# Optimization experiments

Measured on AMD Instinct MI355X. Metric: run time of the kernel, lower is better.

Reference implementation:

```python
import jax, jax.numpy as jnp
import numpy as np

N = 40000      # nodes
E = 640000     # edges (before self-loops)
G = 64         # graphs in batch
H = 4          # heads
C = 64         # channels per head (graph_hidden_channels)
F_IN = 256     # num_node_features
NHID = 1024
NOUT = 768
NEG_SLOPE = 0.2


def setup_inputs() -> dict:
    key = jax.random.key(0)
    ks = jax.random.split(key, 20)
    s = 0.05
    inp = {
        "x": jax.random.normal(ks[0], (N, F_IN), jnp.float32),
        "edge_index": jax.random.randint(ks[1], (2, E), 0, N, dtype=jnp.int64),
        "batch": jnp.sort(jax.random.randint(ks[2], (N,), 0, G, dtype=jnp.int64)),
        # GATConv 1: in F_IN -> H heads x C
        "W1": jax.random.normal(ks[3], (F_IN, H * C), jnp.float32) * s,
        "as1": jax.random.normal(ks[4], (H, C), jnp.float32) * s,
        "ad1": jax.random.normal(ks[5], (H, C), jnp.float32) * s,
        "b1": jnp.zeros((H * C,), jnp.float32),
        # GATConv 2: in H*C -> H x C
        "W2": jax.random.normal(ks[6], (H * C, H * C), jnp.float32) * s,
        "as2": jax.random.normal(ks[7], (H, C), jnp.float32) * s,
        "ad2": jax.random.normal(ks[8], (H, C), jnp.float32) * s,
        "b2": jnp.zeros((H * C,), jnp.float32),
        # GATConv 3
        "W3": jax.random.normal(ks[9], (H * C, H * C), jnp.float32) * s,
        "as3": jax.random.normal(ks[10], (H, C), jnp.float32) * s,
        "ad3": jax.random.normal(ks[11], (H, C), jnp.float32) * s,
        "b3": jnp.zeros((H * C,), jnp.float32),
        # MLP head
        "Wm1": jax.random.normal(ks[12], (H * C, NHID), jnp.float32) * s,
        "bm1": jnp.zeros((NHID,), jnp.float32),
        "Wm2": jax.random.normal(ks[13], (NHID, NOUT), jnp.float32) * s,
        "bm2": jnp.zeros((NOUT,), jnp.float32),
    }
    return inp


def _gat_layer(x, src, dst, W, a_src, a_dst, b):
    """PyG GATConv (concat=True, self-loops already in src/dst)."""
    n = x.shape[0]
    h = (x @ W).reshape(n, H, C)                       # [N,H,C]
    # per-node attention scalars (gather scalars per edge, not full features)
    alpha_src = jnp.einsum('nhc,hc->nh', h, a_src)     # [N,H]
    alpha_dst = jnp.einsum('nhc,hc->nh', h, a_dst)     # [N,H]
    e = alpha_src[src] + alpha_dst[dst]                # [E,H]
    e = jax.nn.leaky_relu(e, NEG_SLOPE)
    # segment softmax over incoming edges of each dst node
    m = jax.ops.segment_max(e, dst, num_segments=n)    # [N,H]
    e = jnp.exp(e - m[dst])
    denom = jax.ops.segment_sum(e, dst, num_segments=n)  # [N,H]; >0 via self-loops
    alpha = e / denom[dst]                             # [E,H]
    # scatter-add weighted source features to destinations
    msg = h[src] * alpha[:, :, None]                   # [E,H,C]
    out = jax.ops.segment_sum(msg, dst, num_segments=n)  # [N,H,C]
    return out.reshape(n, H * C) + b


def reference(x, edge_index, batch,
              W1, as1, ad1, b1,
              W2, as2, ad2, b2,
              W3, as3, ad3, b3,
              Wm1, bm1, Wm2, bm2):
    n = x.shape[0]
    loops = jnp.arange(n, dtype=edge_index.dtype)
    src = jnp.concatenate([edge_index[0], loops])
    dst = jnp.concatenate([edge_index[1], loops])

    h = jax.nn.relu(_gat_layer(x, src, dst, W1, as1, ad1, b1))
    h = jax.nn.relu(_gat_layer(h, src, dst, W2, as2, ad2, b2))
    h = _gat_layer(h, src, dst, W3, as3, ad3, b3)

    # global mean pool over graphs
    sums = jax.ops.segment_sum(h, batch, num_segments=G)      # [G, H*C]
    counts = jax.ops.segment_sum(jnp.ones((n,), h.dtype), batch, num_segments=G)
    pooled = sums / jnp.maximum(counts, 1.0)[:, None]

    out = jax.nn.relu(pooled @ Wm1 + bm1)
    out = out @ Wm2 + bm2
    return out
```

## Files before the change

kernel.cpp:

```cpp
#include <hip/hip_runtime.h>
#include <hip/hip_bf16.h>
#include <math.h>

#define N_NODES 40000
#define N_EDGES 640000
#define N_GRAPH 64
#define HEADS 4
#define CHAN 64
#define HC 256
#define NHID 1024
#define NOUT 768
#define E_TOT (N_EDGES + N_NODES)
#define SCAN_NB ((N_NODES + 255) / 256)

typedef __attribute__((ext_vector_type(8))) short bf16x8;
typedef __attribute__((ext_vector_type(4))) float f32x4;
typedef __attribute__((ext_vector_type(2))) float f32x2;

__device__ inline float bflo(unsigned u) { return __uint_as_float(u << 16); }
__device__ inline float bfhi(unsigned u) { return __uint_as_float(u & 0xffff0000u); }

__device__ inline f32x2 unpk2(unsigned u) {
    return (f32x2){__uint_as_float(u << 16), __uint_as_float(u & 0xffff0000u)};
}
__device__ inline void pkfma(f32x2& a, f32x2 w2, f32x2 h2) {
    asm("v_pk_fma_f32 %0, %1, %2, %0" : "+v"(a) : "v"(w2), "v"(h2));
}

__device__ inline unsigned bfbits(float f) {
    __hip_bfloat16 b = __float2bfloat16(f);
    return (unsigned)*reinterpret_cast<unsigned short*>(&b);
}
__device__ inline unsigned pk2bf(float lo, float hi) {
    return bfbits(lo) | (bfbits(hi) << 16);
}


__global__ void cast_x_kernel(const float* __restrict__ x, __hip_bfloat16* __restrict__ xb) {
    int i = blockIdx.x * blockDim.x + threadIdx.x;
    float4 v = *reinterpret_cast<const float4*>(&x[(size_t)i * 4]);
    __hip_bfloat16 o[4] = {__float2bfloat16(v.x), __float2bfloat16(v.y),
                           __float2bfloat16(v.z), __float2bfloat16(v.w)};
    *reinterpret_cast<ushort4*>(&xb[(size_t)i * 4]) = *reinterpret_cast<ushort4*>(o);
}

__global__ void conv_wt3_kernel(const float* __restrict__ W1, const float* __restrict__ W2,
                                const float* __restrict__ W3, __hip_bfloat16* __restrict__ T1,
                                __hip_bfloat16* __restrict__ T2, __hip_bfloat16* __restrict__ T3) {
    const float* W = (blockIdx.y == 0) ? W1 : (blockIdx.y == 1) ? W2 : W3;
    __hip_bfloat16* T = (blockIdx.y == 0) ? T1 : (blockIdx.y == 1) ? T2 : T3;
    int k = blockIdx.x, n = threadIdx.x;
    T[(size_t)n * 256 + k] = __float2bfloat16(W[(size_t)k * 256 + n]);
}


__global__ void count_deg_kernel(const int* __restrict__ ei, int* __restrict__ deg) {
    int i = blockIdx.x * blockDim.x + threadIdx.x;
    if (i >= E_TOT) return;
    int dst = (i < N_EDGES) ? ei[N_EDGES + i] : (i - N_EDGES);
    atomicAdd(&deg[dst], 1);
}

__global__ __launch_bounds__(256)
void scan_p1_kernel(const int* __restrict__ deg, int* __restrict__ bsum) {
    const int b = blockIdx.x, t = threadIdx.x;
    const int i = b * 256 + t;
    int v = (i < N_NODES) ? deg[i] : 0;
    #pragma unroll
    for (int off = 1; off < 64; off <<= 1) v += __shfl_xor(v, off, 64);
    __shared__ int ws[4];
    if ((t & 63) == 0) ws[t >> 6] = v;
    __syncthreads();
    if (t == 0) bsum[b] = ws[0] + ws[1] + ws[2] + ws[3];
}

__global__ __launch_bounds__(256)
void scan_p2_kernel(int* __restrict__ bsum) {
    __shared__ int s[256];
    const int t = threadIdx.x;
    int v = (t < SCAN_NB) ? bsum[t] : 0;
    s[t] = v;
    __syncthreads();
    #pragma unroll
    for (int off = 1; off < 256; off <<= 1) {
        int x = (t >= off) ? s[t - off] : 0;
        __syncthreads();
        s[t] += x;
        __syncthreads();
    }
    if (t < SCAN_NB) bsum[t] = s[t] - v;
}

__global__ __launch_bounds__(256)
void scan_p3_kernel(const int* __restrict__ deg, const int* __restrict__ bsum,
                    int* __restrict__ rowptr) {
    __shared__ int s[256];
    const int b = blockIdx.x, t = threadIdx.x;
    const int i = b * 256 + t;
    int v = (i < N_NODES) ? deg[i] : 0;
    s[t] = v;
    __syncthreads();
    #pragma unroll
    for (int off = 1; off < 256; off <<= 1) {
        int x = (t >= off) ? s[t - off] : 0;
        __syncthreads();
        s[t] += x;
        __syncthreads();
    }
    if (i < N_NODES) rowptr[i] = bsum[b] + s[t] - v;
    if (i == 0) rowptr[N_NODES] = E_TOT;
}

__global__ void fill_csr_kernel(const int* __restrict__ ei, const int* __restrict__ rowptr,
                                int* __restrict__ cursor, int* __restrict__ csr_src) {
    int i = blockIdx.x * blockDim.x + threadIdx.x;
    if (i >= E_TOT) return;
    int src, dst;
    if (i < N_EDGES) { src = ei[i]; dst = ei[N_EDGES + i]; }
    else             { src = dst = i - N_EDGES; }
    int pos = atomicAdd(&cursor[dst], 1);
    csr_src[rowptr[dst] + pos] = src;
}


__global__ __launch_bounds__(256)
void gemm_mfma_kernel(const __hip_bfloat16* __restrict__ A, const __hip_bfloat16* __restrict__ Wt,
                      __hip_bfloat16* __restrict__ C,
                      const float* __restrict__ a_s, const float* __restrict__ a_d,
                      float* __restrict__ asrc, float* __restrict__ adst) {
    __shared__ __align__(16) union {
        struct { ushort A[64][40]; ushort B[256][40]; } t;
        float strip[4][16][68];
    } lds;

    const int tid = threadIdx.x;
    const int lane = tid & 63;
    const int l15 = lane & 15;
    const int lq  = lane >> 4;
    const int wc  = tid >> 6;
    const int row0 = blockIdx.x * 64;

    const char* Ab = (const char*)A;
    const char* Wb = (const char*)Wt;

    const int ar = tid >> 2;
    const int aq = tid & 3;
    const size_t a_goff = (size_t)(row0 + ar) * 512 + aq * 16;

    f32x4 acc[4][4];
    #pragma unroll
    for (int m = 0; m < 4; m++)
        #pragma unroll
        for (int n = 0; n < 4; n++)
            acc[m][n] = (f32x4){0.f, 0.f, 0.f, 0.f};

    uint4 ra, rb0, rb1, rb2, rb3;
    ra  = *reinterpret_cast<const uint4*>(Ab + a_goff);
    rb0 = *reinterpret_cast<const uint4*>(Wb + (size_t)(ar      ) * 512 + aq * 16);
    rb1 = *reinterpret_cast<const uint4*>(Wb + (size_t)(ar +  64) * 512 + aq * 16);
    rb2 = *reinterpret_cast<const uint4*>(Wb + (size_t)(ar + 128) * 512 + aq * 16);
    rb3 = *reinterpret_cast<const uint4*>(Wb + (size_t)(ar + 192) * 512 + aq * 16);
    *reinterpret_cast<uint4*>(&lds.t.A[ar][aq * 8]) = ra;
    *reinterpret_cast<uint4*>(&lds.t.B[ar][aq * 8]) = rb0;
    *reinterpret_cast<uint4*>(&lds.t.B[ar + 64][aq * 8]) = rb1;
    *reinterpret_cast<uint4*>(&lds.t.B[ar + 128][aq * 8]) = rb2;
    *reinterpret_cast<uint4*>(&lds.t.B[ar + 192][aq * 8]) = rb3;
    __syncthreads();

    for (int kt = 0; kt < 8; ++kt) {
        if (kt < 7) {
            const size_t ko = (size_t)(kt + 1) * 64;
            ra  = *reinterpret_cast<const uint4*>(Ab + a_goff + ko);
            rb0 = *reinterpret_cast<const uint4*>(Wb + (size_t)(ar      ) * 512 + aq * 16 + ko);
            rb1 = *reinterpret_cast<const uint4*>(Wb + (size_t)(ar +  64) * 512 + aq * 16 + ko);
            rb2 = *reinterpret_cast<const uint4*>(Wb + (size_t)(ar + 128) * 512 + aq * 16 + ko);
            rb3 = *reinterpret_cast<const uint4*>(Wb + (size_t)(ar + 192) * 512 + aq * 16 + ko);
        }
        bf16x8 af[4], bfr[4];
        #pragma unroll
        for (int m = 0; m < 4; m++)
            af[m] = *reinterpret_cast<const bf16x8*>(&lds.t.A[m * 16 + l15][lq * 8]);
        #pragma unroll
        for (int n = 0; n < 4; n++)
            bfr[n] = *reinterpret_cast<const bf16x8*>(&lds.t.B[wc * 64 + n * 16 + l15][lq * 8]);
        #pragma unroll
        for (int m = 0; m < 4; m++)
            #pragma unroll
            for (int n = 0; n < 4; n++)
                acc[m][n] = __builtin_amdgcn_mfma_f32_16x16x32_bf16(af[m], bfr[n], acc[m][n], 0, 0, 0);
        __syncthreads();
        if (kt < 7) {
            *reinterpret_cast<uint4*>(&lds.t.A[ar][aq * 8]) = ra;
            *reinterpret_cast<uint4*>(&lds.t.B[ar][aq * 8]) = rb0;
            *reinterpret_cast<uint4*>(&lds.t.B[ar + 64][aq * 8]) = rb1;
            *reinterpret_cast<uint4*>(&lds.t.B[ar + 128][aq * 8]) = rb2;
            *reinterpret_cast<uint4*>(&lds.t.B[ar + 192][aq * 8]) = rb3;
            __syncthreads();
        }
    }

    const int head = wc;
    const int r  = lane >> 2;
    const int cq = lane & 3;
    #pragma unroll
    for (int m = 0; m < 4; m++) {
        #pragma unroll
        for (int n = 0; n < 4; n++)
            #pragma unroll
            for (int reg = 0; reg < 4; reg++)
                lds.strip[wc][lq * 4 + reg][n * 16 + l15] = acc[m][n][reg];
        f32x4 c0 = *reinterpret_cast<const f32x4*>(&lds.strip[wc][r][cq * 16]);
        f32x4 c1 = *reinterpret_cast<const f32x4*>(&lds.strip[wc][r][cq * 16 + 4]);
        f32x4 c2 = *reinterpret_cast<const f32x4*>(&lds.strip[wc][r][cq * 16 + 8]);
        f32x4 c3 = *reinterpret_cast<const f32x4*>(&lds.strip[wc][r][cq * 16 + 12]);
        float ps = 0.f, pd = 0.f;
        #pragma unroll
        for (int k4 = 0; k4 < 4; k4++) {
            f32x4 cv = (k4 == 0) ? c0 : (k4 == 1) ? c1 : (k4 == 2) ? c2 : c3;
            #pragma unroll
            for (int j = 0; j < 4; j++) {
                float wsv = a_s[head * 64 + cq * 16 + k4 * 4 + j];
                float wdv = a_d[head * 64 + cq * 16 + k4 * 4 + j];
                ps = fmaf(cv[j], wsv, ps);
                pd = fmaf(cv[j], wdv, pd);
            }
        }
        ps += __shfl_xor(ps, 1, 4); ps += __shfl_xor(ps, 2, 4);
        pd += __shfl_xor(pd, 1, 4); pd += __shfl_xor(pd, 2, 4);
        const int row = row0 + m * 16 + r;
        if (cq == 0) {
            asrc[row * 4 + head] = ps;
            adst[row * 4 + head] = pd;
        }
        uint4 o0 = make_uint4(pk2bf(c0[0], c0[1]), pk2bf(c0[2], c0[3]),
                              pk2bf(c1[0], c1[1]), pk2bf(c1[2], c1[3]));
        uint4 o1 = make_uint4(pk2bf(c2[0], c2[1]), pk2bf(c2[2], c2[3]),
                              pk2bf(c3[0], c3[1]), pk2bf(c3[2], c3[3]));
        __hip_bfloat16* Cp = C + (size_t)row * 256 + wc * 64 + cq * 16;
        *reinterpret_cast<uint4*>(Cp) = o0;
        *reinterpret_cast<uint4*>(Cp + 8) = o1;
    }
}


#define ACHUNK 256

__global__ __launch_bounds__(256)
void gat_fused_agg(const __hip_bfloat16* __restrict__ h, const float* __restrict__ asrc,
                   const float* __restrict__ adst, const int* __restrict__ rowptr,
                   const int* __restrict__ csr_src, const float* __restrict__ bias,
                   __hip_bfloat16* __restrict__ out, int do_relu) {
    __shared__ int   s_src[ACHUNK];
    __shared__ float s_w[ACHUNK][5];
    __shared__ float s_acc[8][HC];
    __shared__ float s_sum[4];

    const int n = blockIdx.x;
    const int t = threadIdx.x;
    const int lane = t & 63;
    const int wid = t >> 6;
    const int grp = t >> 5;
    const int gl  = t & 31;
    const int h3  = gl >> 3;
    const int start = rowptr[n];
    const int deg = rowptr[n + 1] - start;
    const float ad = adst[n * 4 + wid];

    float ssum = 0.f;
    f32x2 ap0 = {0.f, 0.f}, ap1 = {0.f, 0.f}, ap2 = {0.f, 0.f}, ap3 = {0.f, 0.f};

    for (int c0 = 0; c0 < deg; c0 += ACHUNK) {
        const int cn = min(ACHUNK, deg - c0);
        if (c0) __syncthreads();
        for (int e = lane; e < cn; e += 64) {
            int src = csr_src[start + c0 + e];
            if (wid == 0) s_src[e] = src;
            float sc = asrc[src * 4 + wid] + ad;
            sc = (sc >= 0.f) ? sc : 0.2f * sc;
            float w = __expf(sc);
            s_w[e][wid] = w;
            ssum += w;
        }
        __syncthreads();
        #pragma unroll 2
        for (int e = grp; e < cn; e += 8) {
            float w = s_w[e][h3];
            f32x2 w2 = {w, w};
            uint4 v = *reinterpret_cast<const uint4*>(&h[(size_t)s_src[e] * HC + gl * 8]);
            pkfma(ap0, w2, unpk2(v.x));
            pkfma(ap1, w2, unpk2(v.y));
            pkfma(ap2, w2, unpk2(v.z));
            pkfma(ap3, w2, unpk2(v.w));
        }
    }
    #pragma unroll
    for (int off = 1; off < 64; off <<= 1) ssum += __shfl_xor(ssum, off, 64);
    if (lane == 0) s_sum[wid] = ssum;
    s_acc[grp][gl * 8 + 0] = ap0.x; s_acc[grp][gl * 8 + 1] = ap0.y;
    s_acc[grp][gl * 8 + 2] = ap1.x; s_acc[grp][gl * 8 + 3] = ap1.y;
    s_acc[grp][gl * 8 + 4] = ap2.x; s_acc[grp][gl * 8 + 5] = ap2.y;
    s_acc[grp][gl * 8 + 6] = ap3.x; s_acc[grp][gl * 8 + 7] = ap3.y;
    __syncthreads();
    float tot = 0.f;
    #pragma unroll
    for (int g = 0; g < 8; g++) tot += s_acc[g][t];
    float r = tot / s_sum[t >> 6] + bias[t];
    if (do_relu) r = fmaxf(r, 0.f);
    out[(size_t)n * HC + t] = __float2bfloat16(r);
}


__global__ void graph_bounds_kernel(const int* __restrict__ batch, int* __restrict__ cnt) {
    int g = threadIdx.x;
    if (g >= N_GRAPH) return;
    int lo = 0, hi = N_NODES;
    while (lo < hi) { int mid = (lo + hi) >> 1; if (batch[mid] < g) lo = mid + 1; else hi = mid; }
    int start = lo;
    lo = 0; hi = N_NODES;
    while (lo < hi) { int mid = (lo + hi) >> 1; if (batch[mid] < g + 1) lo = mid + 1; else hi = mid; }
    cnt[g] = lo - start;
}

__global__ __launch_bounds__(256)
void pool_kernel(const __hip_bfloat16* __restrict__ h, const int* __restrict__ batch,
                 float* __restrict__ pooled) {
    __shared__ float s_acc[8][HC];
    const int g = blockIdx.x;
    const int t = threadIdx.x;
    const int grp = t >> 5;
    const int gl  = t & 31;
    int lo = 0, hi = N_NODES;
    while (lo < hi) { int mid = (lo + hi) >> 1; if (batch[mid] < g) lo = mid + 1; else hi = mid; }
    const int start = lo;
    lo = 0; hi = N_NODES;
    while (lo < hi) { int mid = (lo + hi) >> 1; if (batch[mid] < g + 1) lo = mid + 1; else hi = mid; }
    const int end = lo;

    float acc[8] = {0.f, 0.f, 0.f, 0.f, 0.f, 0.f, 0.f, 0.f};
    for (int n = start + grp; n < end; n += 8) {
        uint4 v = *reinterpret_cast<const uint4*>(&h[(size_t)n * HC + gl * 8]);
        acc[0] += bflo(v.x); acc[1] += bfhi(v.x);
        acc[2] += bflo(v.y); acc[3] += bfhi(v.y);
        acc[4] += bflo(v.z); acc[5] += bfhi(v.z);
        acc[6] += bflo(v.w); acc[7] += bfhi(v.w);
    }
    #pragma unroll
    for (int j = 0; j < 8; j++) s_acc[grp][gl * 8 + j] = acc[j];
    __syncthreads();
    float tot = 0.f;
    #pragma unroll
    for (int q = 0; q < 8; q++) tot += s_acc[q][t];
    pooled[g * HC + t] = tot;
}


__global__ __launch_bounds__(1024)
void mlp1_kernel(const float* __restrict__ pooled, const int* __restrict__ cnt,
                 const float* __restrict__ W, const float* __restrict__ b,
                 float* __restrict__ hidden) {
    __shared__ float row[256];
    const int g = blockIdx.x, t = threadIdx.x;
    if (t < 256) {
        float c = (float)max(cnt[g], 1);
        row[t] = pooled[g * 256 + t] / c;
    }
    __syncthreads();
    float acc = b[t];
    for (int k = 0; k < 256; k++) acc = fmaf(row[k], W[(size_t)k * NHID + t], acc);
    hidden[g * NHID + t] = fmaxf(acc, 0.f);
}

__global__ __launch_bounds__(768)
void mlp2_kernel(const float* __restrict__ hidden, const float* __restrict__ W,
                 const float* __restrict__ b, float* __restrict__ out) {
    __shared__ float row[NHID];
    const int g = blockIdx.x, t = threadIdx.x;
    row[t] = hidden[g * NHID + t];
    if (t < NHID - NOUT) row[NOUT + t] = hidden[g * NHID + NOUT + t];
    __syncthreads();
    float acc = b[t];
    for (int k = 0; k < NHID; k++) acc = fmaf(row[k], W[(size_t)k * NOUT + t], acc);
    out[g * NOUT + t] = acc;
}


extern "C" void kernel_launch(void* const* d_in, const int* in_sizes, int n_in,
                              void* d_out, int out_size, void* d_ws, size_t ws_size,
                              hipStream_t stream) {
    const float* x  = (const float*)d_in[0];
    const int* ei   = (const int*)d_in[1];
    const int* batch = (const int*)d_in[2];
    const float* W1 = (const float*)d_in[3];
    const float* as1 = (const float*)d_in[4];
    const float* ad1 = (const float*)d_in[5];
    const float* b1 = (const float*)d_in[6];
    const float* W2 = (const float*)d_in[7];
    const float* as2 = (const float*)d_in[8];
    const float* ad2 = (const float*)d_in[9];
    const float* b2 = (const float*)d_in[10];
    const float* W3 = (const float*)d_in[11];
    const float* as3 = (const float*)d_in[12];
    const float* ad3 = (const float*)d_in[13];
    const float* b3 = (const float*)d_in[14];
    const float* Wm1 = (const float*)d_in[15];
    const float* bm1 = (const float*)d_in[16];
    const float* Wm2 = (const float*)d_in[17];
    const float* bm2 = (const float*)d_in[18];
    float* out = (float*)d_out;

    char* base = (char*)d_ws;
    size_t off = 0;
    auto alloc = [&](size_t bytes) { char* p = base + off; off = (off + bytes + 255) & ~(size_t)255; return p; };
    __hip_bfloat16* x_bf = (__hip_bfloat16*)alloc((size_t)N_NODES * 256 * 2);
    __hip_bfloat16* hA   = (__hip_bfloat16*)alloc((size_t)N_NODES * 256 * 2);
    __hip_bfloat16* hB   = (__hip_bfloat16*)alloc((size_t)N_NODES * 256 * 2);
    __hip_bfloat16* Wt1  = (__hip_bfloat16*)alloc((size_t)256 * 256 * 2);
    __hip_bfloat16* Wt2  = (__hip_bfloat16*)alloc((size_t)256 * 256 * 2);
    __hip_bfloat16* Wt3  = (__hip_bfloat16*)alloc((size_t)256 * 256 * 2);
    float* asrc   = (float*)alloc((size_t)N_NODES * 4 * 4);
    float* adst   = (float*)alloc((size_t)N_NODES * 4 * 4);
    int*   deg    = (int*)alloc((size_t)N_NODES * 4);
    int*   cursor = (int*)alloc((size_t)N_NODES * 4);
    int*   rowptr = (int*)alloc((size_t)(N_NODES + 1) * 4);
    int*   bsum   = (int*)alloc((size_t)SCAN_NB * 4);
    int*   csrsrc = (int*)alloc((size_t)E_TOT * 4);
    float* pooled = (float*)alloc((size_t)N_GRAPH * 256 * 4);
    int*   cnt    = (int*)alloc((size_t)N_GRAPH * 4);
    float* hidden = (float*)alloc((size_t)N_GRAPH * NHID * 4);
    (void)ws_size; (void)n_in; (void)in_sizes; (void)out_size;

    hipMemsetAsync(deg, 0, (size_t)N_NODES * 4, stream);
    hipMemsetAsync(cursor, 0, (size_t)N_NODES * 4, stream);

    cast_x_kernel<<<(N_NODES * 256 / 4 + 255) / 256, 256, 0, stream>>>(x, x_bf);
    conv_wt3_kernel<<<dim3(256, 3), 256, 0, stream>>>(W1, W2, W3, Wt1, Wt2, Wt3);

    const int eb = (E_TOT + 255) / 256;
    count_deg_kernel<<<eb, 256, 0, stream>>>(ei, deg);
    scan_p1_kernel<<<SCAN_NB, 256, 0, stream>>>(deg, bsum);
    scan_p2_kernel<<<1, 256, 0, stream>>>(bsum);
    scan_p3_kernel<<<SCAN_NB, 256, 0, stream>>>(deg, bsum, rowptr);
    fill_csr_kernel<<<eb, 256, 0, stream>>>(ei, rowptr, cursor, csrsrc);

    const int ggrid = N_NODES / 64;

    gemm_mfma_kernel<<<ggrid, 256, 0, stream>>>(x_bf, Wt1, hA, as1, ad1, asrc, adst);
    gat_fused_agg<<<N_NODES, 256, 0, stream>>>(hA, asrc, adst, rowptr, csrsrc, b1, hB, 1);
    gemm_mfma_kernel<<<ggrid, 256, 0, stream>>>(hB, Wt2, hA, as2, ad2, asrc, adst);
    gat_fused_agg<<<N_NODES, 256, 0, stream>>>(hA, asrc, adst, rowptr, csrsrc, b2, hB, 1);
    gemm_mfma_kernel<<<ggrid, 256, 0, stream>>>(hB, Wt3, hA, as3, ad3, asrc, adst);
    gat_fused_agg<<<N_NODES, 256, 0, stream>>>(hA, asrc, adst, rowptr, csrsrc, b3, hB, 0);

    graph_bounds_kernel<<<1, 64, 0, stream>>>(batch, cnt);
    pool_kernel<<<N_GRAPH, 256, 0, stream>>>(hB, batch, pooled);
    mlp1_kernel<<<N_GRAPH, 1024, 0, stream>>>(pooled, cnt, Wm1, bm1, hidden);
    mlp2_kernel<<<N_GRAPH, NOUT, 0, stream>>>(hidden, Wm2, bm2, out);
}
```

Measured before the change: 432.9 us.

## Fuse x cast into GEMM, double-buffer GEMM tiles, merge pool with MLP1

Removes the standalone cast of x to bf16 by converting fp32 rows inside the first GEMM's A-tile load. The GEMM moves to 32-row tiles with double-buffered LDS, which drops one barrier per k-step and doubles the block count. Pooling, graph-bounds and MLP1 are merged into one kernel, the two memsets become one, and the aggregation's packed-FMA asm is replaced with scalar fmaf. Smaller tiles reload the weight matrix more often per row, and the fused pool kernel reads bf16 one element at a time.

Result: faster. 422.1 us (-2.5%).

```diff
diff --git a/kernel.cpp b/kernel.cpp
--- a/kernel.cpp
+++ b/kernel.cpp
@@ -15,17 +15,9 @@
 
 typedef __attribute__((ext_vector_type(8))) short bf16x8;
 typedef __attribute__((ext_vector_type(4))) float f32x4;
-typedef __attribute__((ext_vector_type(2))) float f32x2;
 
 __device__ inline float bflo(unsigned u) { return __uint_as_float(u << 16); }
 __device__ inline float bfhi(unsigned u) { return __uint_as_float(u & 0xffff0000u); }
-
-__device__ inline f32x2 unpk2(unsigned u) {
-    return (f32x2){__uint_as_float(u << 16), __uint_as_float(u & 0xffff0000u)};
-}
-__device__ inline void pkfma(f32x2& a, f32x2 w2, f32x2 h2) {
-    asm("v_pk_fma_f32 %0, %1, %2, %0" : "+v"(a) : "v"(w2), "v"(h2));
-}
 
 __device__ inline unsigned bfbits(float f) {
     __hip_bfloat16 b = __float2bfloat16(f);
@@ -35,14 +27,6 @@
     return bfbits(lo) | (bfbits(hi) << 16);
 }
 
-
-__global__ void cast_x_kernel(const float* __restrict__ x, __hip_bfloat16* __restrict__ xb) {
-    int i = blockIdx.x * blockDim.x + threadIdx.x;
-    float4 v = *reinterpret_cast<const float4*>(&x[(size_t)i * 4]);
-    __hip_bfloat16 o[4] = {__float2bfloat16(v.x), __float2bfloat16(v.y),
-                           __float2bfloat16(v.z), __float2bfloat16(v.w)};
-    *reinterpret_cast<ushort4*>(&xb[(size_t)i * 4]) = *reinterpret_cast<ushort4*>(o);
-}
 
 __global__ void conv_wt3_kernel(const float* __restrict__ W1, const float* __restrict__ W2,
                                 const float* __restrict__ W3, __hip_bfloat16* __restrict__ T1,
@@ -123,78 +107,95 @@
 }
 
 
+template<int CAST>
 __global__ __launch_bounds__(256)
-void gemm_mfma_kernel(const __hip_bfloat16* __restrict__ A, const __hip_bfloat16* __restrict__ Wt,
+void gemm_mfma_kernel(const void* __restrict__ Ain, const __hip_bfloat16* __restrict__ Wt,
                       __hip_bfloat16* __restrict__ C,
                       const float* __restrict__ a_s, const float* __restrict__ a_d,
                       float* __restrict__ asrc, float* __restrict__ adst) {
     __shared__ __align__(16) union {
-        struct { ushort A[64][40]; ushort B[256][40]; } t;
+        struct { ushort A0[32][32]; ushort B0[256][32]; ushort A1[32][32]; ushort B1[256][32]; } t;
         float strip[4][16][68];
     } lds;
 
     const int tid = threadIdx.x;
     const int lane = tid & 63;
-    const int l15 = lane & 15;
-    const int lq  = lane >> 4;
+    const int l15 = lane & 15, lq = lane >> 4;
     const int wc  = tid >> 6;
-    const int row0 = blockIdx.x * 64;
-
-    const char* Ab = (const char*)A;
+    const int row0 = blockIdx.x * 32;
     const char* Wb = (const char*)Wt;
-
-    const int ar = tid >> 2;
-    const int aq = tid & 3;
-    const size_t a_goff = (size_t)(row0 + ar) * 512 + aq * 16;
-
-    f32x4 acc[4][4];
-    #pragma unroll
-    for (int m = 0; m < 4; m++)
+    const int br = tid >> 2;
+    const int bq = tid & 3;
+
+    f32x4 acc[2][4];
+    #pragma unroll
+    for (int m = 0; m < 2; m++)
         #pragma unroll
         for (int n = 0; n < 4; n++)
             acc[m][n] = (f32x4){0.f, 0.f, 0.f, 0.f};
 
-    uint4 ra, rb0, rb1, rb2, rb3;
-    ra  = *reinterpret_cast<const uint4*>(Ab + a_goff);
-    rb0 = *reinterpret_cast<const uint4*>(Wb + (size_t)(ar      ) * 512 + aq * 16);
-    rb1 = *reinterpret_cast<const uint4*>(Wb + (size_t)(ar +  64) * 512 + aq * 16);
-    rb2 = *reinterpret_cast<const uint4*>(Wb + (size_t)(ar + 128) * 512 + aq * 16);
-    rb3 = *reinterpret_cast<const uint4*>(Wb + (size_t)(ar + 192) * 512 + aq * 16);
-    *reinterpret_cast<uint4*>(&lds.t.A[ar][aq * 8]) = ra;
-    *reinterpret_cast<uint4*>(&lds.t.B[ar][aq * 8]) = rb0;
-    *reinterpret_cast<uint4*>(&lds.t.B[ar + 64][aq * 8]) = rb1;
-    *reinterpret_cast<uint4*>(&lds.t.B[ar + 128][aq * 8]) = rb2;
-    *reinterpret_cast<uint4*>(&lds.t.B[ar + 192][aq * 8]) = rb3;
-    __syncthreads();
+    {
+        #pragma unroll
+        for (int c = 0; c < 4; c++) {
+            uint4 v = *reinterpret_cast<const uint4*>(Wb + (size_t)(c * 64 + br) * 512 + bq * 16);
+            *reinterpret_cast<uint4*>(&lds.t.B0[c * 64 + br][bq * 8]) = v;
+        }
+        if (CAST) {
+            const float* Af = (const float*)Ain;
+            float4 v = *reinterpret_cast<const float4*>(&Af[(size_t)(row0 + (tid >> 3)) * 256 + (tid & 7) * 4]);
+            uint2 w = make_uint2(pk2bf(v.x, v.y), pk2bf(v.z, v.w));
+            *reinterpret_cast<uint2*>((ushort*)lds.t.A0 + tid * 4) = w;
+        } else if (tid < 128) {
+            const char* Ab = (const char*)Ain;
+            uint4 v = *reinterpret_cast<const uint4*>(Ab + (size_t)(row0 + (tid >> 2)) * 512 + (tid & 3) * 16);
+            *reinterpret_cast<uint4*>((ushort*)lds.t.A0 + tid * 8) = v;
+        }
+        __syncthreads();
+    }
 
     for (int kt = 0; kt < 8; ++kt) {
+        ushort (*Acur)[32] = (kt & 1) ? lds.t.A1 : lds.t.A0;
+        ushort (*Bcur)[32] = (kt & 1) ? lds.t.B1 : lds.t.B0;
+        bf16x8 af[2], bfr[4];
+        #pragma unroll
+        for (int m = 0; m < 2; m++)
+            af[m] = *reinterpret_cast<const bf16x8*>(&Acur[m * 16 + l15][lq * 8]);
+        #pragma unroll
+        for (int n = 0; n < 4; n++)
+            bfr[n] = *reinterpret_cast<const bf16x8*>(&Bcur[wc * 64 + n * 16 + l15][lq * 8]);
+        uint4 rb0, rb1, rb2, rb3, ra; float4 rf;
         if (kt < 7) {
             const size_t ko = (size_t)(kt + 1) * 64;
-            ra  = *reinterpret_cast<const uint4*>(Ab + a_goff + ko);
-            rb0 = *reinterpret_cast<const uint4*>(Wb + (size_t)(ar      ) * 512 + aq * 16 + ko);
-            rb1 = *reinterpret_cast<const uint4*>(Wb + (size_t)(ar +  64) * 512 + aq * 16 + ko);
-            rb2 = *reinterpret_cast<const uint4*>(Wb + (size_t)(ar + 128) * 512 + aq * 16 + ko);
-            rb3 = *reinterpret_cast<const uint4*>(Wb + (size_t)(ar + 192) * 512 + aq * 16 + ko);
-        }
-        bf16x8 af[4], bfr[4];
-        #pragma unroll
-        for (int m = 0; m < 4; m++)
-            af[m] = *reinterpret_cast<const bf16x8*>(&lds.t.A[m * 16 + l15][lq * 8]);
-        #pragma unroll
-        for (int n = 0; n < 4; n++)
-            bfr[n] = *reinterpret_cast<const bf16x8*>(&lds.t.B[wc * 64 + n * 16 + l15][lq * 8]);
-        #pragma unroll
-        for (int m = 0; m < 4; m++)
+            rb0 = *reinterpret_cast<const uint4*>(Wb + (size_t)(      br) * 512 + bq * 16 + ko);
+            rb1 = *reinterpret_cast<const uint4*>(Wb + (size_t)( 64 + br) * 512 + bq * 16 + ko);
+            rb2 = *reinterpret_cast<const uint4*>(Wb + (size_t)(128 + br) * 512 + bq * 16 + ko);
+            rb3 = *reinterpret_cast<const uint4*>(Wb + (size_t)(192 + br) * 512 + bq * 16 + ko);
+            if (CAST) {
+                const float* Af = (const float*)Ain;
+                rf = *reinterpret_cast<const float4*>(&Af[(size_t)(row0 + (tid >> 3)) * 256 + (kt + 1) * 32 + (tid & 7) * 4]);
+            } else if (tid < 128) {
+                const char* Ab = (const char*)Ain;
+                ra = *reinterpret_cast<const uint4*>(Ab + (size_t)(row0 + (tid >> 2)) * 512 + (tid & 3) * 16 + ko);
+            }
+        }
+        #pragma unroll
+        for (int m = 0; m < 2; m++)
             #pragma unroll
             for (int n = 0; n < 4; n++)
                 acc[m][n] = __builtin_amdgcn_mfma_f32_16x16x32_bf16(af[m], bfr[n], acc[m][n], 0, 0, 0);
-        __syncthreads();
         if (kt < 7) {
-            *reinterpret_cast<uint4*>(&lds.t.A[ar][aq * 8]) = ra;
-            *reinterpret_cast<uint4*>(&lds.t.B[ar][aq * 8]) = rb0;
-            *reinterpret_cast<uint4*>(&lds.t.B[ar + 64][aq * 8]) = rb1;
-            *reinterpret_cast<uint4*>(&lds.t.B[ar + 128][aq * 8]) = rb2;
-            *reinterpret_cast<uint4*>(&lds.t.B[ar + 192][aq * 8]) = rb3;
+            ushort (*Anx)[32] = (kt & 1) ? lds.t.A0 : lds.t.A1;
+            ushort (*Bnx)[32] = (kt & 1) ? lds.t.B0 : lds.t.B1;
+            *reinterpret_cast<uint4*>(&Bnx[      br][bq * 8]) = rb0;
+            *reinterpret_cast<uint4*>(&Bnx[ 64 + br][bq * 8]) = rb1;
+            *reinterpret_cast<uint4*>(&Bnx[128 + br][bq * 8]) = rb2;
+            *reinterpret_cast<uint4*>(&Bnx[192 + br][bq * 8]) = rb3;
+            if (CAST) {
+                uint2 w = make_uint2(pk2bf(rf.x, rf.y), pk2bf(rf.z, rf.w));
+                *reinterpret_cast<uint2*>((ushort*)Anx + tid * 4) = w;
+            } else if (tid < 128) {
+                *reinterpret_cast<uint4*>((ushort*)Anx + tid * 8) = ra;
+            }
             __syncthreads();
         }
     }
@@ -203,7 +204,7 @@
     const int r  = lane >> 2;
     const int cq = lane & 3;
     #pragma unroll
-    for (int m = 0; m < 4; m++) {
+    for (int m = 0; m < 2; m++) {
         #pragma unroll
         for (int n = 0; n < 4; n++)
             #pragma unroll
@@ -219,10 +220,8 @@
             f32x4 cv = (k4 == 0) ? c0 : (k4 == 1) ? c1 : (k4 == 2) ? c2 : c3;
             #pragma unroll
             for (int j = 0; j < 4; j++) {
-                float wsv = a_s[head * 64 + cq * 16 + k4 * 4 + j];
-                float wdv = a_d[head * 64 + cq * 16 + k4 * 4 + j];
-                ps = fmaf(cv[j], wsv, ps);
-                pd = fmaf(cv[j], wdv, pd);
+                ps = fmaf(cv[j], a_s[head * 64 + cq * 16 + k4 * 4 + j], ps);
+                pd = fmaf(cv[j], a_d[head * 64 + cq * 16 + k4 * 4 + j], pd);
             }
         }
         ps += __shfl_xor(ps, 1, 4); ps += __shfl_xor(ps, 2, 4);
@@ -267,7 +266,7 @@
     const float ad = adst[n * 4 + wid];
 
     float ssum = 0.f;
-    f32x2 ap0 = {0.f, 0.f}, ap1 = {0.f, 0.f}, ap2 = {0.f, 0.f}, ap3 = {0.f, 0.f};
+    float acc[8] = {0.f, 0.f, 0.f, 0.f, 0.f, 0.f, 0.f, 0.f};
 
     for (int c0 = 0; c0 < deg; c0 += ACHUNK) {
         const int cn = min(ACHUNK, deg - c0);
@@ -285,21 +284,22 @@
         #pragma unroll 2
         for (int e = grp; e < cn; e += 8) {
             float w = s_w[e][h3];
-            f32x2 w2 = {w, w};
             uint4 v = *reinterpret_cast<const uint4*>(&h[(size_t)s_src[e] * HC + gl * 8]);
-            pkfma(ap0, w2, unpk2(v.x));
-            pkfma(ap1, w2, unpk2(v.y));
-            pkfma(ap2, w2, unpk2(v.z));
-            pkfma(ap3, w2, unpk2(v.w));
+            acc[0] = fmaf(w, bflo(v.x), acc[0]);
+            acc[1] = fmaf(w, bfhi(v.x), acc[1]);
+            acc[2] = fmaf(w, bflo(v.y), acc[2]);
+            acc[3] = fmaf(w, bfhi(v.y), acc[3]);
+            acc[4] = fmaf(w, bflo(v.z), acc[4]);
+            acc[5] = fmaf(w, bfhi(v.z), acc[5]);
+            acc[6] = fmaf(w, bflo(v.w), acc[6]);
+            acc[7] = fmaf(w, bfhi(v.w), acc[7]);
         }
     }
     #pragma unroll
     for (int off = 1; off < 64; off <<= 1) ssum += __shfl_xor(ssum, off, 64);
     if (lane == 0) s_sum[wid] = ssum;
-    s_acc[grp][gl * 8 + 0] = ap0.x; s_acc[grp][gl * 8 + 1] = ap0.y;
-    s_acc[grp][gl * 8 + 2] = ap1.x; s_acc[grp][gl * 8 + 3] = ap1.y;
-    s_acc[grp][gl * 8 + 4] = ap2.x; s_acc[grp][gl * 8 + 5] = ap2.y;
-    s_acc[grp][gl * 8 + 6] = ap3.x; s_acc[grp][gl * 8 + 7] = ap3.y;
+    *reinterpret_cast<float4*>(&s_acc[grp][gl * 8])     = make_float4(acc[0], acc[1], acc[2], acc[3]);
+    *reinterpret_cast<float4*>(&s_acc[grp][gl * 8 + 4]) = make_float4(acc[4], acc[5], acc[6], acc[7]);
     __syncthreads();
     float tot = 0.f;
     #pragma unroll
@@ -310,25 +310,13 @@
 }
 
 
-__global__ void graph_bounds_kernel(const int* __restrict__ batch, int* __restrict__ cnt) {
-    int g = threadIdx.x;
-    if (g >= N_GRAPH) return;
-    int lo = 0, hi = N_NODES;
-    while (lo < hi) { int mid = (lo + hi) >> 1; if (batch[mid] < g) lo = mid + 1; else hi = mid; }
-    int start = lo;
-    lo = 0; hi = N_NODES;
-    while (lo < hi) { int mid = (lo + hi) >> 1; if (batch[mid] < g + 1) lo = mid + 1; else hi = mid; }
-    cnt[g] = lo - start;
-}
-
-__global__ __launch_bounds__(256)
-void pool_kernel(const __hip_bfloat16* __restrict__ h, const int* __restrict__ batch,
-                 float* __restrict__ pooled) {
-    __shared__ float s_acc[8][HC];
-    const int g = blockIdx.x;
-    const int t = threadIdx.x;
-    const int grp = t >> 5;
-    const int gl  = t & 31;
+__global__ __launch_bounds__(1024)
+void pool_mlp1_kernel(const __hip_bfloat16* __restrict__ h, const int* __restrict__ batch,
+                      const float* __restrict__ Wm1, const float* __restrict__ bm1,
+                      float* __restrict__ hidden) {
+    __shared__ float s_part[4][256];
+    __shared__ float row[256];
+    const int g = blockIdx.x, t = threadIdx.x;
     int lo = 0, hi = N_NODES;
     while (lo < hi) { int mid = (lo + hi) >> 1; if (batch[mid] < g) lo = mid + 1; else hi = mid; }
     const int start = lo;
@@ -336,38 +324,20 @@
     while (lo < hi) { int mid = (lo + hi) >> 1; if (batch[mid] < g + 1) lo = mid + 1; else hi = mid; }
     const int end = lo;
 
-    float acc[8] = {0.f, 0.f, 0.f, 0.f, 0.f, 0.f, 0.f, 0.f};
-    for (int n = start + grp; n < end; n += 8) {
-        uint4 v = *reinterpret_cast<const uint4*>(&h[(size_t)n * HC + gl * 8]);
-        acc[0] += bflo(v.x); acc[1] += bfhi(v.x);
-        acc[2] += bflo(v.y); acc[3] += bfhi(v.y);
-        acc[4] += bflo(v.z); acc[5] += bfhi(v.z);
-        acc[6] += bflo(v.w); acc[7] += bfhi(v.w);
-    }
-    #pragma unroll
-    for (int j = 0; j < 8; j++) s_acc[grp][gl * 8 + j] = acc[j];
-    __syncthreads();
-    float tot = 0.f;
-    #pragma unroll
-    for (int q = 0; q < 8; q++) tot += s_acc[q][t];
-    pooled[g * HC + t] = tot;
-}
-
-
-__global__ __launch_bounds__(1024)
-void mlp1_kernel(const float* __restrict__ pooled, const int* __restrict__ cnt,
-                 const float* __restrict__ W, const float* __restrict__ b,
-                 float* __restrict__ hidden) {
-    __shared__ float row[256];
-    const int g = blockIdx.x, t = threadIdx.x;
+    const int sub = t >> 8, ch = t & 255;
+    float a = 0.f;
+    for (int n = start + sub; n < end; n += 4)
+        a += __bfloat162float(h[(size_t)n * HC + ch]);
+    s_part[sub][ch] = a;
+    __syncthreads();
     if (t < 256) {
-        float c = (float)max(cnt[g], 1);
-        row[t] = pooled[g * 256 + t] / c;
-    }
-    __syncthreads();
-    float acc = b[t];
-    for (int k = 0; k < 256; k++) acc = fmaf(row[k], W[(size_t)k * NHID + t], acc);
-    hidden[g * NHID + t] = fmaxf(acc, 0.f);
+        float c = (float)max(end - start, 1);
+        row[t] = (s_part[0][t] + s_part[1][t] + s_part[2][t] + s_part[3][t]) / c;
+    }
+    __syncthreads();
+    float acc = bm1[t];
+    for (int k = 0; k < 256; k++) acc = fmaf(row[k], Wm1[(size_t)k * NHID + t], acc);
+    hidden[(size_t)g * NHID + t] = fmaxf(acc, 0.f);
 }
 
 __global__ __launch_bounds__(768)
@@ -411,7 +381,6 @@
     char* base = (char*)d_ws;
     size_t off = 0;
     auto alloc = [&](size_t bytes) { char* p = base + off; off = (off + bytes + 255) & ~(size_t)255; return p; };
-    __hip_bfloat16* x_bf = (__hip_bfloat16*)alloc((size_t)N_NODES * 256 * 2);
     __hip_bfloat16* hA   = (__hip_bfloat16*)alloc((size_t)N_NODES * 256 * 2);
     __hip_bfloat16* hB   = (__hip_bfloat16*)alloc((size_t)N_NODES * 256 * 2);
     __hip_bfloat16* Wt1  = (__hip_bfloat16*)alloc((size_t)256 * 256 * 2);
@@ -424,15 +393,11 @@
     int*   rowptr = (int*)alloc((size_t)(N_NODES + 1) * 4);
     int*   bsum   = (int*)alloc((size_t)SCAN_NB * 4);
     int*   csrsrc = (int*)alloc((size_t)E_TOT * 4);
-    float* pooled = (float*)alloc((size_t)N_GRAPH * 256 * 4);
-    int*   cnt    = (int*)alloc((size_t)N_GRAPH * 4);
     float* hidden = (float*)alloc((size_t)N_GRAPH * NHID * 4);
     (void)ws_size; (void)n_in; (void)in_sizes; (void)out_size;
 
-    hipMemsetAsync(deg, 0, (size_t)N_NODES * 4, stream);
-    hipMemsetAsync(cursor, 0, (size_t)N_NODES * 4, stream);
-
-    cast_x_kernel<<<(N_NODES * 256 / 4 + 255) / 256, 256, 0, stream>>>(x, x_bf);
+    hipMemsetAsync(deg, 0, (size_t)N_NODES * 4 * 2, stream);
+
     conv_wt3_kernel<<<dim3(256, 3), 256, 0, stream>>>(W1, W2, W3, Wt1, Wt2, Wt3);
 
     const int eb = (E_TOT + 255) / 256;
@@ -442,17 +407,15 @@
     scan_p3_kernel<<<SCAN_NB, 256, 0, stream>>>(deg, bsum, rowptr);
     fill_csr_kernel<<<eb, 256, 0, stream>>>(ei, rowptr, cursor, csrsrc);
 
-    const int ggrid = N_NODES / 64;
-
-    gemm_mfma_kernel<<<ggrid, 256, 0, stream>>>(x_bf, Wt1, hA, as1, ad1, asrc, adst);
+    const int ggrid = N_NODES / 32;
+
+    gemm_mfma_kernel<1><<<ggrid, 256, 0, stream>>>(x, Wt1, hA, as1, ad1, asrc, adst);
     gat_fused_agg<<<N_NODES, 256, 0, stream>>>(hA, asrc, adst, rowptr, csrsrc, b1, hB, 1);
-    gemm_mfma_kernel<<<ggrid, 256, 0, stream>>>(hB, Wt2, hA, as2, ad2, asrc, adst);
+    gemm_mfma_kernel<0><<<ggrid, 256, 0, stream>>>(hB, Wt2, hA, as2, ad2, asrc, adst);
     gat_fused_agg<<<N_NODES, 256, 0, stream>>>(hA, asrc, adst, rowptr, csrsrc, b2, hB, 1);
-    gemm_mfma_kernel<<<ggrid, 256, 0, stream>>>(hB, Wt3, hA, as3, ad3, asrc, adst);
+    gemm_mfma_kernel<0><<<ggrid, 256, 0, stream>>>(hB, Wt3, hA, as3, ad3, asrc, adst);
     gat_fused_agg<<<N_NODES, 256, 0, stream>>>(hA, asrc, adst, rowptr, csrsrc, b3, hB, 0);
 
-    graph_bounds_kernel<<<1, 64, 0, stream>>>(batch, cnt);
-    pool_kernel<<<N_GRAPH, 256, 0, stream>>>(hB, batch, pooled);
-    mlp1_kernel<<<N_GRAPH, 1024, 0, stream>>>(pooled, cnt, Wm1, bm1, hidden);
+    pool_mlp1_kernel<<<N_GRAPH, 1024, 0, stream>>>(hB, batch, Wm1, bm1, hidden);
     mlp2_kernel<<<N_GRAPH, NOUT, 0, stream>>>(hidden, Wm2, bm2, out);
 }
```
